# Performance work log

Measured on AMD Instinct MI355X. Metric: run time of the kernel, lower is better.

Reference implementation:

```python
import jax, jax.numpy as jnp
import numpy as np

F = 128
E = 100000   # num_edges
T = 1000000  # num_triplets


def setup_inputs() -> dict:
    key = jax.random.key(0)
    ks = jax.random.split(key, 20)
    s = 0.05
    return {
        "f": jax.random.normal(ks[0], (E, 2 * F), jnp.float32),
        "M01": jax.random.normal(ks[1], (T, F), jnp.float32),
        "M02": jax.random.normal(ks[2], (T, F), jnp.float32),
        # split_net MLP([2F, 2F, 2F]): Linear -> act -> Linear
        "W1": jax.random.normal(ks[3], (2 * F, 2 * F), jnp.float32) * s,
        "b1": jnp.zeros((2 * F,), jnp.float32),
        "W2": jax.random.normal(ks[4], (2 * F, 2 * F), jnp.float32) * s,
        "b2": jnp.zeros((2 * F,), jnp.float32),
        "Ws01": jax.random.normal(ks[5], (F, F), jnp.float32) * s,
        "bs01": jnp.zeros((F,), jnp.float32),
        "Ws02": jax.random.normal(ks[6], (F, F), jnp.float32) * s,
        "bs02": jnp.zeros((F,), jnp.float32),
        "Ws": jax.random.normal(ks[7], (2 * F, F), jnp.float32) * s,
        "bs": jnp.zeros((F,), jnp.float32),
        "Wout": jax.random.normal(ks[8], (F, F), jnp.float32) * s,
        "bout": jnp.zeros((F,), jnp.float32),
        "num_edges": E,
        "idx_ji": jax.random.randint(ks[9], (T,), 0, E, jnp.int32),
        "idx_ki": jax.random.randint(ks[10], (T,), 0, E, jnp.int32),
    }


def reference(f, M01, M02, W1, b1, W2, b2, Ws01, bs01, Ws02, bs02, Ws, bs,
              Wout, bout, num_edges, idx_ji, idx_ki):
    act = jax.nn.silu
    # f = act(split_net(f)); split_net = Linear -> act -> Linear
    h = act(act(f @ W1 + b1) @ W2 + b2)          # [E, 2F]
    f01, f02 = jnp.split(h, 2, axis=-1)           # [E, F] each
    # triplet interaction: gather -> multiply -> linear -> act
    s01 = act((f01[idx_ki] * M01 * f01[idx_ji]) @ Ws01 + bs01)  # [T, F]
    s02 = act((f02[idx_ki] * M02 * f02[idx_ji]) @ Ws02 + bs02)  # [T, F]
    s = act(jnp.concatenate((s01, s02), axis=-1) @ Ws + bs)     # [T, F]
    # scatter-sum triplets back to edges
    out = jax.ops.segment_sum(s, idx_ji, num_segments=num_edges)  # [E, F]
    return out @ Wout + bout
```

## Files before the change

### kernel.cpp

```cpp
#include <hip/hip_runtime.h>

typedef __attribute__((ext_vector_type(8))) short short8;
typedef __attribute__((ext_vector_type(4))) float f32x4;

__device__ __forceinline__ float silu_f(float x) { return x / (1.0f + __expf(-x)); }

__device__ __forceinline__ unsigned short f2bf(float x) {
  unsigned u = __float_as_uint(x);
  u += 0x7FFFu + ((u >> 16) & 1u);
  return (unsigned short)(u >> 16);
}
__device__ __forceinline__ float bf2f(unsigned short v) {
  return __uint_as_float(((unsigned)v) << 16);
}
__device__ __forceinline__ unsigned cvtpk_bf16(float lo, float hi) {
  unsigned r;
  asm("v_cvt_pk_bf16_f32 %0, %1, %2" : "=v"(r) : "v"(lo), "v"(hi));
  return r;
}

#define LGKM_SB() do { asm volatile("s_waitcnt lgkmcnt(0)" ::: "memory"); \
                       __builtin_amdgcn_sched_barrier(0); } while (0)

__device__ __forceinline__ void prep_one(const float* __restrict__ W,
                                         unsigned short* __restrict__ wh,
                                         unsigned short* __restrict__ wl,
                                         int N, int e)
{
  int k = e / N, n = e % N;
  float w = W[e];
  unsigned short hi = f2bf(w);
  unsigned short lo = f2bf(w - bf2f(hi));
  int kp = k >> 6, kk = k & 63;
  size_t dst = (size_t)kp * N * 64 + (size_t)n * 64 + ((((kk >> 3) ^ (n & 7)) << 3)) + (kk & 7);
  wh[dst] = hi;
  wl[dst] = lo;
}

__global__ void prep_all(const float* __restrict__ W1, unsigned short* w1h, unsigned short* w1l,
                         const float* __restrict__ W2, unsigned short* w2h, unsigned short* w2l,
                         const float* __restrict__ Wo, unsigned short* woh, unsigned short* wol,
                         const int* __restrict__ ji, int* __restrict__ cnt, int T)
{
  int e = blockIdx.x * 256 + threadIdx.x;
  if (e < 256 * 256) {
    prep_one(W1, w1h, w1l, 256, e);
    prep_one(W2, w2h, w2l, 256, e);
  }
  if (e < 128 * 128) prep_one(Wo, woh, wol, 128, e);
  const int stride = gridDim.x * 256;
  for (int t = e; t < T; t += stride) atomicAdd(&cnt[ji[t]], 1);
}

template<int INBF, int ASPLIT>
__global__ __launch_bounds__(512)
void mlp_gemm(const void* A_, const unsigned short* __restrict__ wh,
              const unsigned short* __restrict__ wl,
              const float* __restrict__ bias, unsigned short* __restrict__ C, int M)
{
  __shared__ unsigned short aTh[64 * 64], aTl[64 * 64];
  __shared__ unsigned short whb[256 * 64], wlb[256 * 64];
  const int tid = threadIdx.x;
  const int lane = tid & 63, wv = tid >> 6;
  const int g = wv & 3, hh = wv >> 2;
  const int l15 = lane & 15, l4 = lane >> 4;
  const int row0 = blockIdx.x * 64;
  const int r = tid >> 3, kseg = (tid & 7) * 8;
  const f32x4 zero4 = {0.f, 0.f, 0.f, 0.f};

  f32x4 acc[8];
#pragma unroll
  for (int nt = 0; nt < 8; nt++) acc[nt] = zero4;

  for (int kp = 0; kp < 4; kp++) {
    {
      const int grow = row0 + r;
      float x[8];
      if (grow < M) {
        if (INBF) {
          short8 v = *(const short8*)((const unsigned short*)A_ + (size_t)grow * 256 + kp * 64 + kseg);
#pragma unroll
          for (int j = 0; j < 8; j++) x[j] = bf2f((unsigned short)v[j]);
        } else {
          const float* ap = (const float*)A_ + (size_t)grow * 256 + kp * 64 + kseg;
          float4 v0 = *(const float4*)ap;
          float4 v1 = *(const float4*)(ap + 4);
          x[0] = v0.x; x[1] = v0.y; x[2] = v0.z; x[3] = v0.w;
          x[4] = v1.x; x[5] = v1.y; x[6] = v1.z; x[7] = v1.w;
        }
      } else {
#pragma unroll
        for (int j = 0; j < 8; j++) x[j] = 0.f;
      }
      union { short8 s; unsigned short us[8]; } H, L;
#pragma unroll
      for (int j = 0; j < 8; j++) {
        H.us[j] = f2bf(x[j]);
        L.us[j] = ASPLIT ? f2bf(x[j] - bf2f(H.us[j])) : (unsigned short)0;
      }
      const int dst = r * 64 + ((((kseg >> 3) ^ (r & 7)) << 3));
      *(short8*)(aTh + dst) = H.s;
      if (ASPLIT) *(short8*)(aTl + dst) = L.s;
    }
    {
      const short8* srcH = (const short8*)(wh + (size_t)kp * 16384);
      const short8* srcL = (const short8*)(wl + (size_t)kp * 16384);
#pragma unroll
      for (int i = 0; i < 4; i++) {
        ((short8*)whb)[tid + 512 * i] = srcH[tid + 512 * i];
        ((short8*)wlb)[tid + 512 * i] = srcL[tid + 512 * i];
      }
    }
    __syncthreads();
#pragma unroll
    for (int ks = 0; ks < 2; ks++) {
      const int arow = 16 * g + l15;
      const int aof = arow * 64 + (((4 * ks + l4) ^ (arow & 7)) << 3);
      short8 ah = *(const short8*)(aTh + aof);
      short8 al = *(const short8*)(aTl + aof);
#pragma unroll
      for (int nt = 0; nt < 8; nt++) {
        const int col = 128 * hh + 16 * nt + l15;
        const int bof = col * 64 + (((4 * ks + l4) ^ (col & 7)) << 3);
        short8 bh = *(const short8*)(whb + bof);
        short8 bl = *(const short8*)(wlb + bof);
        acc[nt] = __builtin_amdgcn_mfma_f32_16x16x32_bf16(ah, bh, acc[nt], 0, 0, 0);
        acc[nt] = __builtin_amdgcn_mfma_f32_16x16x32_bf16(ah, bl, acc[nt], 0, 0, 0);
        if (ASPLIT)
          acc[nt] = __builtin_amdgcn_mfma_f32_16x16x32_bf16(al, bh, acc[nt], 0, 0, 0);
      }
    }
    __syncthreads();
  }
#pragma unroll
  for (int nt = 0; nt < 8; nt++) {
    const int col = 128 * hh + 16 * nt + l15;
    const float bv = bias[col];
#pragma unroll
    for (int i = 0; i < 4; i++) {
      const int row = row0 + 16 * g + 4 * l4 + i;
      if (row < M) C[(size_t)row * 256 + col] = f2bf(silu_f(acc[nt][i] + bv));
    }
  }
}

__global__ __launch_bounds__(512)
void final_gemm(const float* __restrict__ A, const unsigned short* __restrict__ wh,
                const unsigned short* __restrict__ wl,
                const float* __restrict__ bias, float* __restrict__ C, int M)
{
  __shared__ unsigned short aTh[64 * 64], aTl[64 * 64];
  __shared__ unsigned short whb[128 * 64], wlb[128 * 64];
  const int tid = threadIdx.x;
  const int lane = tid & 63, wv = tid >> 6;
  const int g = wv & 3, hh = wv >> 2;
  const int l15 = lane & 15, l4 = lane >> 4;
  const int row0 = blockIdx.x * 64;
  const int r = tid >> 3, kseg = (tid & 7) * 8;
  const f32x4 zero4 = {0.f, 0.f, 0.f, 0.f};

  f32x4 acc[4];
#pragma unroll
  for (int nt = 0; nt < 4; nt++) acc[nt] = zero4;

  for (int kp = 0; kp < 2; kp++) {
    {
      const int grow = row0 + r;
      float x[8];
      if (grow < M) {
        const float* ap = A + (size_t)grow * 128 + kp * 64 + kseg;
        float4 v0 = *(const float4*)ap;
        float4 v1 = *(const float4*)(ap + 4);
        x[0] = v0.x; x[1] = v0.y; x[2] = v0.z; x[3] = v0.w;
        x[4] = v1.x; x[5] = v1.y; x[6] = v1.z; x[7] = v1.w;
      } else {
#pragma unroll
        for (int j = 0; j < 8; j++) x[j] = 0.f;
      }
      union { short8 s; unsigned short us[8]; } H, L;
#pragma unroll
      for (int j = 0; j < 8; j++) {
        H.us[j] = f2bf(x[j]);
        L.us[j] = f2bf(x[j] - bf2f(H.us[j]));
      }
      const int dst = r * 64 + ((((kseg >> 3) ^ (r & 7)) << 3));
      *(short8*)(aTh + dst) = H.s;
      *(short8*)(aTl + dst) = L.s;
    }
    {
      const short8* srcH = (const short8*)(wh + (size_t)kp * 8192);
      const short8* srcL = (const short8*)(wl + (size_t)kp * 8192);
#pragma unroll
      for (int i = 0; i < 2; i++) {
        ((short8*)whb)[tid + 512 * i] = srcH[tid + 512 * i];
        ((short8*)wlb)[tid + 512 * i] = srcL[tid + 512 * i];
      }
    }
    __syncthreads();
#pragma unroll
    for (int ks = 0; ks < 2; ks++) {
      const int arow = 16 * g + l15;
      const int aof = arow * 64 + (((4 * ks + l4) ^ (arow & 7)) << 3);
      short8 ah = *(const short8*)(aTh + aof);
      short8 al = *(const short8*)(aTl + aof);
#pragma unroll
      for (int nt = 0; nt < 4; nt++) {
        const int col = 64 * hh + 16 * nt + l15;
        const int bof = col * 64 + (((4 * ks + l4) ^ (col & 7)) << 3);
        short8 bh = *(const short8*)(whb + bof);
        short8 bl = *(const short8*)(wlb + bof);
        acc[nt] = __builtin_amdgcn_mfma_f32_16x16x32_bf16(ah, bh, acc[nt], 0, 0, 0);
        acc[nt] = __builtin_amdgcn_mfma_f32_16x16x32_bf16(ah, bl, acc[nt], 0, 0, 0);
        acc[nt] = __builtin_amdgcn_mfma_f32_16x16x32_bf16(al, bh, acc[nt], 0, 0, 0);
      }
    }
    __syncthreads();
  }
#pragma unroll
  for (int nt = 0; nt < 4; nt++) {
    const int col = 64 * hh + 16 * nt + l15;
    const float bv = bias[col];
#pragma unroll
    for (int i = 0; i < 4; i++) {
      const int row = row0 + 16 * g + 4 * l4 + i;
      if (row < M) C[(size_t)row * 128 + col] = acc[nt][i] + bv;
    }
  }
}

__global__ void scan1_k(const int* __restrict__ cnt, int* __restrict__ csum, int E) {
  __shared__ int red[256];
  const int c0 = blockIdx.x * 2048;
  int s = 0;
  for (int i = threadIdx.x; i < 2048; i += 256) {
    int e = c0 + i;
    if (e < E) s += cnt[e];
  }
  red[threadIdx.x] = s;
  __syncthreads();
  for (int o = 128; o > 0; o >>= 1) {
    if (threadIdx.x < o) red[threadIdx.x] += red[threadIdx.x + o];
    __syncthreads();
  }
  if (threadIdx.x == 0) csum[blockIdx.x] = red[0];
}

__global__ void scan2_k(int* __restrict__ csum, int n) {
  const int lane = threadIdx.x;
  int v = (lane < n) ? csum[lane] : 0;
  const int orig = v;
  for (int o = 1; o < 64; o <<= 1) {
    int t = __shfl_up(v, o, 64);
    if (lane >= o) v += t;
  }
  if (lane < n) csum[lane] = v - orig;
}

__global__ void scan3_k(const int* __restrict__ cnt, const int* __restrict__ csum,
                        int* __restrict__ off, int E) {
  __shared__ int ts[256];
  const int c0 = blockIdx.x * 2048;
  const int tid = threadIdx.x;
  int loc[8];
  int s = 0;
#pragma unroll
  for (int k = 0; k < 8; k++) {
    int e = c0 + tid * 8 + k;
    loc[k] = (e < E) ? cnt[e] : 0;
    s += loc[k];
  }
  ts[tid] = s;
  __syncthreads();
  for (int o = 1; o < 256; o <<= 1) {
    int v = (tid >= o) ? ts[tid - o] : 0;
    __syncthreads();
    ts[tid] += v;
    __syncthreads();
  }
  int base = csum[blockIdx.x] + ((tid > 0) ? ts[tid - 1] : 0);
#pragma unroll
  for (int k = 0; k < 8; k++) {
    int e = c0 + tid * 8 + k;
    if (e < E) { off[e] = base; base += loc[k]; }
  }
}

__global__ void scatter_k(const int* __restrict__ ji, int* __restrict__ cursor,
                          int* __restrict__ perm, int T) {
  int t = blockIdx.x * 256 + threadIdx.x;
  const int stride = gridDim.x * 256;
  for (; t < T; t += stride) {
    int e = ji[t];
    int p = atomicAdd(&cursor[e], 1);
    perm[p] = t;
  }
}

__device__ __forceinline__ short8 pack8p(const short8 a, const short8 b,
                                         const float4 m0, const float4 m1)
{
  float p0 = bf2f((unsigned short)a[0]) * m0.x * bf2f((unsigned short)b[0]);
  float p1 = bf2f((unsigned short)a[1]) * m0.y * bf2f((unsigned short)b[1]);
  float p2 = bf2f((unsigned short)a[2]) * m0.z * bf2f((unsigned short)b[2]);
  float p3 = bf2f((unsigned short)a[3]) * m0.w * bf2f((unsigned short)b[3]);
  float p4 = bf2f((unsigned short)a[4]) * m1.x * bf2f((unsigned short)b[4]);
  float p5 = bf2f((unsigned short)a[5]) * m1.y * bf2f((unsigned short)b[5]);
  float p6 = bf2f((unsigned short)a[6]) * m1.z * bf2f((unsigned short)b[6]);
  float p7 = bf2f((unsigned short)a[7]) * m1.w * bf2f((unsigned short)b[7]);
  union { short8 s; unsigned u[4]; } t;
  t.u[0] = cvtpk_bf16(p0, p1);
  t.u[1] = cvtpk_bf16(p2, p3);
  t.u[2] = cvtpk_bf16(p4, p5);
  t.u[3] = cvtpk_bf16(p6, p7);
  return t.s;
}

__global__ __launch_bounds__(512, 2)
void triplet_fused(const unsigned short* __restrict__ h,
                   const float* __restrict__ M01, const float* __restrict__ M02,
                   const float* __restrict__ Ws01, const float* __restrict__ bs01,
                   const float* __restrict__ Ws02, const float* __restrict__ bs02,
                   const float* __restrict__ Ws,   const float* __restrict__ bs,
                   const int* __restrict__ idx_ji, const int* __restrict__ idx_ki,
                   const int* __restrict__ perm,
                   float* __restrict__ out_acc, int T)
{
  __shared__ unsigned short wF01[16384];
  __shared__ unsigned short wF02[16384];
  __shared__ unsigned short wFA[16384];
  __shared__ unsigned short wFB[16384];
  __shared__ unsigned short sbuf[8][2048];

  const int tid = threadIdx.x;
  for (int e = tid; e < 16384; e += 512) {
    const int j = e & 7, ln = (e >> 3) & 63, ks = (e >> 9) & 3, ct = e >> 11;
    const int col = 16 * ct + (ln & 15);
    const int k = 32 * ks + 8 * (ln >> 4) + j;
    const int src = k * 128 + col;
    wF01[e] = f2bf(Ws01[src]);
    wF02[e] = f2bf(Ws02[src]);
    wFA[e]  = f2bf(Ws[src]);
    wFB[e]  = f2bf(Ws[16384 + src]);
  }
  __syncthreads();

  const int lane = tid & 63, wv = tid >> 6;
  const int l15 = lane & 15, l4 = lane >> 4;
  unsigned short* const sb = sbuf[wv];
  const f32x4 zero4 = {0.f, 0.f, 0.f, 0.f};

  float bs01v[8], bs02v[8], bsv[8];
#pragma unroll
  for (int ct = 0; ct < 8; ct++) {
    bs01v[ct] = bs01[16 * ct + l15];
    bs02v[ct] = bs02[16 * ct + l15];
    bsv[ct]   = bs[16 * ct + l15];
  }

  const int nsub = T >> 4;
  const int stride = gridDim.x * 8;
  int sub = blockIdx.x * 8 + wv;

  int pidx = perm[(sub << 4) + l15];
  int ek = idx_ki[pidx], ej = idx_ji[pidx];

  for (; sub < nsub; sub += stride) {
    const unsigned short* fa = h + (size_t)ek * 256 + 8 * l4;
    const unsigned short* fb = h + (size_t)ej * 256 + 8 * l4;
    const float* mm1 = M01 + (size_t)pidx * 128 + 8 * l4;
    const float* mm2 = M02 + (size_t)pidx * 128 + 8 * l4;
    short8 ra1[4], rb1[4], ra2[4], rb2[4];
    float4 rm1[8], rm2[8];
#pragma unroll
    for (int ks = 0; ks < 4; ks++) {
      ra1[ks] = *(const short8*)(fa + 32 * ks);
      rb1[ks] = *(const short8*)(fb + 32 * ks);
      rm1[2 * ks]     = *(const float4*)(mm1 + 32 * ks);
      rm1[2 * ks + 1] = *(const float4*)(mm1 + 32 * ks + 4);
      ra2[ks] = *(const short8*)(fa + 128 + 32 * ks);
      rb2[ks] = *(const short8*)(fb + 128 + 32 * ks);
      rm2[2 * ks]     = *(const float4*)(mm2 + 32 * ks);
      rm2[2 * ks + 1] = *(const float4*)(mm2 + 32 * ks + 4);
    }

    const int subn = sub + stride;
    int sidx = (subn << 4) + l15;
    if (sidx >= T) sidx = T - 1;
    const int pidx_n = perm[sidx];

    f32x4 acc1[8];
#pragma unroll
    for (int ct = 0; ct < 8; ct++) acc1[ct] = zero4;
    __builtin_amdgcn_s_setprio(1);
#pragma unroll
    for (int ks = 0; ks < 4; ks++) {
      const short8 a = pack8p(ra1[ks], rb1[ks], rm1[2 * ks], rm1[2 * ks + 1]);
#pragma unroll
      for (int ct = 0; ct < 8; ct++) {
        const short8 b = *(const short8*)(wF01 + ((ct * 4 + ks) * 64 + lane) * 8);
        acc1[ct] = __builtin_amdgcn_mfma_f32_16x16x32_bf16(a, b, acc1[ct], 0, 0, 0);
      }
    }
    __builtin_amdgcn_s_setprio(0);

#pragma unroll
    for (int ct = 0; ct < 8; ct++) {
      const int chi = 2 * ct + (l15 >> 3);
#pragma unroll
      for (int i = 0; i < 4; i++) {
        const int row = 4 * l4 + i;
        sb[row * 128 + (((chi ^ (row & 7)) << 3)) + (l15 & 7)] =
            f2bf(silu_f(acc1[ct][i] + bs01v[ct]));
      }
    }
    LGKM_SB();
    short8 as1[4];
#pragma unroll
    for (int ks = 0; ks < 4; ks++)
      as1[ks] = *(const short8*)(sb + l15 * 128 + (((4 * ks + l4) ^ (l15 & 7)) << 3));

    f32x4 acc3[8];
#pragma unroll
    for (int ct = 0; ct < 8; ct++) acc3[ct] = zero4;
    __builtin_amdgcn_s_setprio(1);
#pragma unroll
    for (int ks = 0; ks < 4; ks++)
#pragma unroll
      for (int ct = 0; ct < 8; ct++) {
        const short8 b = *(const short8*)(wFA + ((ct * 4 + ks) * 64 + lane) * 8);
        acc3[ct] = __builtin_amdgcn_mfma_f32_16x16x32_bf16(as1[ks], b, acc3[ct], 0, 0, 0);
      }
    __builtin_amdgcn_s_setprio(0);

    const int ekn = idx_ki[pidx_n], ejn = idx_ji[pidx_n];

#pragma unroll
    for (int ct = 0; ct < 8; ct++) acc1[ct] = zero4;
    __builtin_amdgcn_s_setprio(1);
#pragma unroll
    for (int ks = 0; ks < 4; ks++) {
      const short8 a = pack8p(ra2[ks], rb2[ks], rm2[2 * ks], rm2[2 * ks + 1]);
#pragma unroll
      for (int ct = 0; ct < 8; ct++) {
        const short8 b = *(const short8*)(wF02 + ((ct * 4 + ks) * 64 + lane) * 8);
        acc1[ct] = __builtin_amdgcn_mfma_f32_16x16x32_bf16(a, b, acc1[ct], 0, 0, 0);
      }
    }
    __builtin_amdgcn_s_setprio(0);

#pragma unroll
    for (int ct = 0; ct < 8; ct++) {
      const int chi = 2 * ct + (l15 >> 3);
#pragma unroll
      for (int i = 0; i < 4; i++) {
        const int row = 4 * l4 + i;
        sb[row * 128 + (((chi ^ (row & 7)) << 3)) + (l15 & 7)] =
            f2bf(silu_f(acc1[ct][i] + bs02v[ct]));
      }
    }
    LGKM_SB();
    short8 as2[4];
#pragma unroll
    for (int ks = 0; ks < 4; ks++)
      as2[ks] = *(const short8*)(sb + l15 * 128 + (((4 * ks + l4) ^ (l15 & 7)) << 3));

    __builtin_amdgcn_s_setprio(1);
#pragma unroll
    for (int ks = 0; ks < 4; ks++)
#pragma unroll
      for (int ct = 0; ct < 8; ct++) {
        const short8 b = *(const short8*)(wFB + ((ct * 4 + ks) * 64 + lane) * 8);
        acc3[ct] = __builtin_amdgcn_mfma_f32_16x16x32_bf16(as2[ks], b, acc3[ct], 0, 0, 0);
      }
    __builtin_amdgcn_s_setprio(0);

#pragma unroll
    for (int ct = 0; ct < 8; ct++)
#pragma unroll
      for (int i = 0; i < 4; i++)
        acc3[ct][i] = silu_f(acc3[ct][i] + bsv[ct]);

    {
      const int ejp = __shfl_up(ej, 1, 16);
      unsigned bm = (unsigned)(__ballot((l15 > 0) && (ej != ejp)) & 0xFFFFull);
      int fr = 0;
      unsigned rem = bm;
      while (fr < 16) {
        const int nxt = rem ? (__ffs(rem) - 1) : 16;
        rem &= rem - 1;
        const int lr = nxt - 1;
        const int e = __shfl(ej, fr, 16);
        float sv[8];
#pragma unroll
        for (int ct = 0; ct < 8; ct++) {
          float s = 0.f;
#pragma unroll
          for (int i = 0; i < 4; i++) {
            const int rr = 4 * l4 + i;
            s += (rr >= fr && rr <= lr) ? acc3[ct][i] : 0.f;
          }
          s += __shfl_xor(s, 16);
          s += __shfl_xor(s, 32);
          sv[ct] = s;
        }
        float w0, w1;
        if (l4 == 0)      { w0 = sv[0]; w1 = sv[1]; }
        else if (l4 == 1) { w0 = sv[2]; w1 = sv[3]; }
        else if (l4 == 2) { w0 = sv[4]; w1 = sv[5]; }
        else              { w0 = sv[6]; w1 = sv[7]; }
        float* dst = out_acc + (size_t)e * 128 + 32 * l4 + l15;
        if (fr == 0 || lr == 15) {
          atomicAdd(dst, w0);
          atomicAdd(dst + 16, w1);
        } else {
          dst[0] = w0;
          dst[16] = w1;
        }
        fr = nxt;
      }
    }

    pidx = pidx_n; ek = ekn; ej = ejn;
  }
}

extern "C" void kernel_launch(void* const* d_in, const int* in_sizes, int n_in,
                              void* d_out, int out_size, void* d_ws, size_t ws_size,
                              hipStream_t stream)
{
  const float* f    = (const float*)d_in[0];
  const float* M01  = (const float*)d_in[1];
  const float* M02  = (const float*)d_in[2];
  const float* W1   = (const float*)d_in[3];
  const float* b1   = (const float*)d_in[4];
  const float* W2   = (const float*)d_in[5];
  const float* b2   = (const float*)d_in[6];
  const float* Ws01 = (const float*)d_in[7];
  const float* bs01 = (const float*)d_in[8];
  const float* Ws02 = (const float*)d_in[9];
  const float* bs02 = (const float*)d_in[10];
  const float* Ws   = (const float*)d_in[11];
  const float* bs   = (const float*)d_in[12];
  const float* Wout = (const float*)d_in[13];
  const float* bout = (const float*)d_in[14];
  const int* idx_ji = (const int*)d_in[16];
  const int* idx_ki = (const int*)d_in[17];

  const int E = in_sizes[0] / 256;
  const int T = in_sizes[1] / 128;

  char* w = (char*)d_ws;
  unsigned short* hbuf = (unsigned short*)w;
  size_t o = ((size_t)E * 256 * 2 + 255) & ~(size_t)255;
  unsigned short* wt1h = (unsigned short*)(w + o); o += 256 * 256 * 2;
  unsigned short* wt1l = (unsigned short*)(w + o); o += 256 * 256 * 2;
  unsigned short* wt2h = (unsigned short*)(w + o); o += 256 * 256 * 2;
  unsigned short* wt2l = (unsigned short*)(w + o); o += 256 * 256 * 2;
  unsigned short* wtoh = (unsigned short*)(w + o); o += 128 * 128 * 2;
  unsigned short* wtol = (unsigned short*)(w + o); o += 128 * 128 * 2;
  o = (o + 255) & ~(size_t)255;
  int* cnt = (int*)(w + o);  o += ((size_t)E * 4 + 255) & ~(size_t)255;
  int* off = (int*)(w + o);  o += ((size_t)E * 4 + 255) & ~(size_t)255;
  int* csum = (int*)(w + o); o += 4096;
  int* perm = (int*)(w + o);

  float* out_acc = (float*)d_out;
  const int mb = (E + 63) / 64;

  hipMemsetAsync(cnt, 0, (size_t)E * 4, stream);
  prep_all<<<(256 * 256 + 255) / 256, 256, 0, stream>>>(W1, wt1h, wt1l,
                                                        W2, wt2h, wt2l,
                                                        Wout, wtoh, wtol,
                                                        idx_ji, cnt, T);

  mlp_gemm<0, 1><<<mb, 512, 0, stream>>>(f, wt1h, wt1l, b1, hbuf, E);
  mlp_gemm<1, 0><<<mb, 512, 0, stream>>>(hbuf, wt2h, wt2l, b2, hbuf, E);

  const int nchunks = (E + 2047) / 2048;
  scan1_k<<<nchunks, 256, 0, stream>>>(cnt, csum, E);
  scan2_k<<<1, 64, 0, stream>>>(csum, nchunks);
  scan3_k<<<nchunks, 256, 0, stream>>>(cnt, csum, off, E);
  scatter_k<<<1024, 256, 0, stream>>>(idx_ji, off, perm, T);

  hipMemsetAsync(d_out, 0, (size_t)E * 128 * sizeof(float), stream);

  triplet_fused<<<256, 512, 0, stream>>>(hbuf, M01, M02, Ws01, bs01, Ws02, bs02,
                                         Ws, bs, idx_ji, idx_ki, perm, out_acc, T);

  final_gemm<<<mb, 512, 0, stream>>>(out_acc, wtoh, wtol, bout, out_acc, E);
}
```

Measured before the change: 777.9 us.

## Prefetch next triplet gathers during scatter, fold scan2 and output memset into other kernels

Result: no change. 792.6 us (+1.9%).

```diff
diff --git a/kernel.cpp b/kernel.cpp
--- a/kernel.cpp
+++ b/kernel.cpp
@@ -245,22 +245,21 @@
   if (threadIdx.x == 0) csum[blockIdx.x] = red[0];
 }
 
-__global__ void scan2_k(int* __restrict__ csum, int n) {
-  const int lane = threadIdx.x;
-  int v = (lane < n) ? csum[lane] : 0;
-  const int orig = v;
-  for (int o = 1; o < 64; o <<= 1) {
-    int t = __shfl_up(v, o, 64);
-    if (lane >= o) v += t;
-  }
-  if (lane < n) csum[lane] = v - orig;
-}
-
 __global__ void scan3_k(const int* __restrict__ cnt, const int* __restrict__ csum,
-                        int* __restrict__ off, int E) {
+                        int* __restrict__ off, int E, int nchunks) {
   __shared__ int ts[256];
+  __shared__ int base_sh;
   const int c0 = blockIdx.x * 2048;
   const int tid = threadIdx.x;
+  if (tid < 64) {
+    int v = (tid < nchunks) ? csum[tid] : 0;
+    for (int o = 1; o < 64; o <<= 1) {
+      int t = __shfl_up(v, o, 64);
+      if (tid >= o) v += t;
+    }
+    if (blockIdx.x == 0) { if (tid == 0) base_sh = 0; }
+    else if (tid == blockIdx.x - 1) base_sh = v;
+  }
   int loc[8];
   int s = 0;
 #pragma unroll
@@ -277,7 +276,7 @@
     ts[tid] += v;
     __syncthreads();
   }
-  int base = csum[blockIdx.x] + ((tid > 0) ? ts[tid - 1] : 0);
+  int base = base_sh + ((tid > 0) ? ts[tid - 1] : 0);
 #pragma unroll
   for (int k = 0; k < 8; k++) {
     int e = c0 + tid * 8 + k;
@@ -286,9 +285,12 @@
 }
 
 __global__ void scatter_k(const int* __restrict__ ji, int* __restrict__ cursor,
-                          int* __restrict__ perm, int T) {
+                          int* __restrict__ perm, int T,
+                          float4* __restrict__ out_zero, int n4) {
   int t = blockIdx.x * 256 + threadIdx.x;
   const int stride = gridDim.x * 256;
+  const float4 z4 = {0.f, 0.f, 0.f, 0.f};
+  for (int i = t; i < n4; i += stride) out_zero[i] = z4;
   for (; t < T; t += stride) {
     int e = ji[t];
     int p = atomicAdd(&cursor[e], 1);
@@ -315,6 +317,31 @@
   return t.s;
 }
 
+__device__ __forceinline__ void issue_g(const unsigned short* __restrict__ h,
+                                        const float* __restrict__ M01,
+                                        const float* __restrict__ M02,
+                                        int ek, int ej, int pidx, int l4,
+                                        short8 (&ra1)[4], short8 (&rb1)[4],
+                                        short8 (&ra2)[4], short8 (&rb2)[4],
+                                        float4 (&rm1)[8], float4 (&rm2)[8])
+{
+  const unsigned short* fa = h + (size_t)ek * 256 + 8 * l4;
+  const unsigned short* fb = h + (size_t)ej * 256 + 8 * l4;
+  const float* mm1 = M01 + (size_t)pidx * 128 + 8 * l4;
+  const float* mm2 = M02 + (size_t)pidx * 128 + 8 * l4;
+#pragma unroll
+  for (int ks = 0; ks < 4; ks++) {
+    ra1[ks] = *(const short8*)(fa + 32 * ks);
+    rb1[ks] = *(const short8*)(fb + 32 * ks);
+    rm1[2 * ks]     = *(const float4*)(mm1 + 32 * ks);
+    rm1[2 * ks + 1] = *(const float4*)(mm1 + 32 * ks + 4);
+    ra2[ks] = *(const short8*)(fa + 128 + 32 * ks);
+    rb2[ks] = *(const short8*)(fb + 128 + 32 * ks);
+    rm2[2 * ks]     = *(const float4*)(mm2 + 32 * ks);
+    rm2[2 * ks + 1] = *(const float4*)(mm2 + 32 * ks + 4);
+  }
+}
+
 __global__ __launch_bounds__(512, 2)
 void triplet_fused(const unsigned short* __restrict__ h,
                    const float* __restrict__ M01, const float* __restrict__ M02,
@@ -362,27 +389,12 @@
   int sub = blockIdx.x * 8 + wv;
 
   int pidx = perm[(sub << 4) + l15];
-  int ek = idx_ki[pidx], ej = idx_ji[pidx];
+  int ej = idx_ji[pidx];
+  short8 ra1[4], rb1[4], ra2[4], rb2[4];
+  float4 rm1[8], rm2[8];
+  issue_g(h, M01, M02, idx_ki[pidx], ej, pidx, l4, ra1, rb1, ra2, rb2, rm1, rm2);
 
   for (; sub < nsub; sub += stride) {
-    const unsigned short* fa = h + (size_t)ek * 256 + 8 * l4;
-    const unsigned short* fb = h + (size_t)ej * 256 + 8 * l4;
-    const float* mm1 = M01 + (size_t)pidx * 128 + 8 * l4;
-    const float* mm2 = M02 + (size_t)pidx * 128 + 8 * l4;
-    short8 ra1[4], rb1[4], ra2[4], rb2[4];
-    float4 rm1[8], rm2[8];
-#pragma unroll
-    for (int ks = 0; ks < 4; ks++) {
-      ra1[ks] = *(const short8*)(fa + 32 * ks);
-      rb1[ks] = *(const short8*)(fb + 32 * ks);
-      rm1[2 * ks]     = *(const float4*)(mm1 + 32 * ks);
-      rm1[2 * ks + 1] = *(const float4*)(mm1 + 32 * ks + 4);
-      ra2[ks] = *(const short8*)(fa + 128 + 32 * ks);
-      rb2[ks] = *(const short8*)(fb + 128 + 32 * ks);
-      rm2[2 * ks]     = *(const float4*)(mm2 + 32 * ks);
-      rm2[2 * ks + 1] = *(const float4*)(mm2 + 32 * ks + 4);
-    }
-
     const int subn = sub + stride;
     int sidx = (subn << 4) + l15;
     if (sidx >= T) sidx = T - 1;
@@ -479,6 +491,8 @@
 #pragma unroll
       for (int i = 0; i < 4; i++)
         acc3[ct][i] = silu_f(acc3[ct][i] + bsv[ct]);
+
+    issue_g(h, M01, M02, ekn, ejn, pidx_n, l4, ra1, rb1, ra2, rb2, rm1, rm2);
 
     {
       const int ejp = __shfl_up(ej, 1, 16);
@@ -520,7 +534,7 @@
       }
     }
 
-    pidx = pidx_n; ek = ekn; ej = ejn;
+    pidx = pidx_n; ej = ejn;
   }
 }
 
@@ -578,11 +592,9 @@
 
   const int nchunks = (E + 2047) / 2048;
   scan1_k<<<nchunks, 256, 0, stream>>>(cnt, csum, E);
-  scan2_k<<<1, 64, 0, stream>>>(csum, nchunks);
-  scan3_k<<<nchunks, 256, 0, stream>>>(cnt, csum, off, E);
-  scatter_k<<<1024, 256, 0, stream>>>(idx_ji, off, perm, T);
-
-  hipMemsetAsync(d_out, 0, (size_t)E * 128 * sizeof(float), stream);
+  scan3_k<<<nchunks, 256, 0, stream>>>(cnt, csum, off, E, nchunks);
+  scatter_k<<<1024, 256, 0, stream>>>(idx_ji, off, perm, T,
+                                      (float4*)out_acc, E * 128 / 4);
 
   triplet_fused<<<256, 512, 0, stream>>>(hbuf, M01, M02, Ws01, bs01, Ws02, bs02,
                                          Ws, bs, idx_ji, idx_ki, perm, out_acc, T);
```
